# Optimization experiments

Measured on AMD Instinct MI355X. Metric: run time of the kernel, lower is better.

The kernel has to match this reference:

```python
import jax, jax.numpy as jnp
import numpy as np


def setup_inputs() -> dict:
    key = jax.random.key(0)
    k1, k2, k3, k4 = jax.random.split(key, 4)
    B, IN, OUT, K = 1024, 1024, 1024, 100
    return {
        "x": jax.random.normal(k1, (B, IN), dtype=jnp.float32),
        "eps": jax.random.normal(k2, (K, IN, OUT), dtype=jnp.float32),
        "weights_m": jax.random.normal(k3, (IN, OUT), dtype=jnp.float32),
        "weights_s": jax.random.normal(k4, (IN, OUT), dtype=jnp.float32),
    }


def reference(x, eps, weights_m, weights_s):
    # Reparameterized Gaussian weight samples: [K, in, out]
    sampled = eps * jax.nn.softplus(weights_s) + weights_m
    # einsum('ij,kjl->kil'): preds [K, B, out]
    preds = jnp.einsum('ij,kjl->kil', x, sampled)
    return preds.mean(0)
```

## Files before the change

### kernel.cpp

```cpp
#include <hip/hip_runtime.h>
#include <cmath>

#define KSAMP 100
#define DIN   1024
#define DOUT  1024
#define DB    1024

typedef float f4 __attribute__((ext_vector_type(4)));

__global__ __launch_bounds__(256) void weff_kernel(
    const f4* __restrict__ eps,
    const f4* __restrict__ wm,
    const f4* __restrict__ ws,
    f4* __restrict__ weff)
{
    const int idx = blockIdx.x * blockDim.x + threadIdx.x;
    const int n4 = (DIN * DOUT) / 4;

    f4 acc0 = {0.f, 0.f, 0.f, 0.f};
    f4 acc1 = {0.f, 0.f, 0.f, 0.f};
    const f4* p = eps + idx;
    #pragma unroll 10
    for (int k = 0; k < KSAMP; k += 2) {
        f4 e0 = __builtin_nontemporal_load(p);
        f4 e1 = __builtin_nontemporal_load(p + n4);
        p += 2 * n4;
        acc0 += e0;
        acc1 += e1;
    }
    f4 sum = acc0 + acc1;

    f4 s = ws[idx];
    f4 m = wm[idx];
    const float invK = 1.0f / (float)KSAMP;

    f4 sp;
    sp.x = fmaxf(s.x, 0.f) + log1pf(expf(-fabsf(s.x)));
    sp.y = fmaxf(s.y, 0.f) + log1pf(expf(-fabsf(s.y)));
    sp.z = fmaxf(s.z, 0.f) + log1pf(expf(-fabsf(s.z)));
    sp.w = fmaxf(s.w, 0.f) + log1pf(expf(-fabsf(s.w)));

    f4 o;
    o.x = fmaf(sum.x * invK, sp.x, m.x);
    o.y = fmaf(sum.y * invK, sp.y, m.y);
    o.z = fmaf(sum.z * invK, sp.z, m.z);
    o.w = fmaf(sum.w * invK, sp.w, m.w);
    weff[idx] = o;
}

#define BM 128
#define BN 128
#define BK 8
#define KSPLIT 8

__global__ __launch_bounds__(256, 2) void sgemm_splitk(
    const float* __restrict__ A,
    const float* __restrict__ B,
    float* __restrict__ P)
{
    __shared__ float As[BK][BM];
    __shared__ float Bs[BK][BN];

    const int bx = blockIdx.x, by = blockIdx.y, kz = blockIdx.z;
    const int tid = threadIdx.x;
    const int tx = tid & 15;
    const int ty = tid >> 4;

    const int kc = DIN / KSPLIT;
    const int k_begin = kz * kc;

    const int arow = tid >> 1;
    const int acol = (tid & 1) * 4;
    const int brow = tid >> 5;
    const int bcol = (tid & 31) * 4;

    const float* Aptr = &A[(size_t)(by * BM + arow) * DIN + k_begin + acol];
    const float* Bptr = &B[(size_t)(k_begin + brow) * DOUT + bx * BN + bcol];

    float acc[8][8];
    #pragma unroll
    for (int i = 0; i < 8; ++i)
        #pragma unroll
        for (int j = 0; j < 8; ++j) acc[i][j] = 0.f;

    float4 a = *(const float4*)Aptr;
    float4 b = *(const float4*)Bptr;

    const int niter = kc / BK;
    for (int it = 0; it < niter; ++it) {
        __syncthreads();
        As[acol + 0][arow] = a.x;
        As[acol + 1][arow] = a.y;
        As[acol + 2][arow] = a.z;
        As[acol + 3][arow] = a.w;
        *(float4*)&Bs[brow][bcol] = b;
        __syncthreads();

        if (it + 1 < niter) {
            a = *(const float4*)(Aptr + (it + 1) * BK);
            b = *(const float4*)(Bptr + (size_t)(it + 1) * BK * DOUT);
        }

        #pragma unroll
        for (int kk = 0; kk < BK; ++kk) {
            float4 a0 = *(const float4*)&As[kk][ty * 8];
            float4 a1 = *(const float4*)&As[kk][ty * 8 + 4];
            float4 b0 = *(const float4*)&Bs[kk][tx * 8];
            float4 b1 = *(const float4*)&Bs[kk][tx * 8 + 4];
            const float ar[8] = {a0.x, a0.y, a0.z, a0.w, a1.x, a1.y, a1.z, a1.w};
            const float br[8] = {b0.x, b0.y, b0.z, b0.w, b1.x, b1.y, b1.z, b1.w};
            #pragma unroll
            for (int i = 0; i < 8; ++i)
                #pragma unroll
                for (int j = 0; j < 8; ++j)
                    acc[i][j] = fmaf(ar[i], br[j], acc[i][j]);
        }
    }

    float* Pz = P + (size_t)kz * DB * DOUT;
    #pragma unroll
    for (int i = 0; i < 8; ++i) {
        const int r = by * BM + ty * 8 + i;
        float* prow = &Pz[(size_t)r * DOUT + bx * BN + tx * 8];
        *(float4*)&prow[0] = make_float4(acc[i][0], acc[i][1], acc[i][2], acc[i][3]);
        *(float4*)&prow[4] = make_float4(acc[i][4], acc[i][5], acc[i][6], acc[i][7]);
    }
}

__global__ __launch_bounds__(256) void reduce_kernel(
    const f4* __restrict__ P, f4* __restrict__ out)
{
    const int idx = blockIdx.x * blockDim.x + threadIdx.x;
    const int n4 = (DB * DOUT) / 4;
    f4 s = P[idx];
    #pragma unroll
    for (int z = 1; z < KSPLIT; ++z) {
        s += P[(size_t)z * n4 + idx];
    }
    out[idx] = s;
}

extern "C" void kernel_launch(void* const* d_in, const int* in_sizes, int n_in,
                              void* d_out, int out_size, void* d_ws, size_t ws_size,
                              hipStream_t stream) {
    const float* x   = (const float*)d_in[0];
    const float* eps = (const float*)d_in[1];
    const float* wm  = (const float*)d_in[2];
    const float* ws  = (const float*)d_in[3];

    float* weff     = (float*)d_ws;
    float* partials = (float*)d_ws + (size_t)DIN * DOUT;

    weff_kernel<<<(DIN * DOUT / 4) / 256, 256, 0, stream>>>(
        (const f4*)eps, (const f4*)wm, (const f4*)ws, (f4*)weff);

    sgemm_splitk<<<dim3(DOUT / BN, DB / BM, KSPLIT), 256, 0, stream>>>(
        x, weff, partials);

    reduce_kernel<<<(DB * DOUT / 4) / 256, 256, 0, stream>>>(
        (const f4*)partials, (f4*)d_out);
}
```

Measured before the change: 585.5 us.

## Fuse split-K reduction into GEMM via last-block atomic counter, widen BK

Removes the separate reduce kernel. Each GEMM block now bumps a per-tile atomic counter after writing its partial, and the last-arriving block sums the eight partials into the output. The weff kernel resets the counters, and its ws/wm loads are hoisted ahead of the eps loop. BK grows from 8 to 16, and the B-tile columns are split into two 64-wide halves to change the LDS access pattern. This saves a kernel launch and part of the partial traffic, at the cost of a serialized tail reduction done by a few blocks plus threadfence overhead.

Result: slower. 628.7 us (+7.4%).

```diff
diff --git a/kernel.cpp b/kernel.cpp
--- a/kernel.cpp
+++ b/kernel.cpp
@@ -12,10 +12,16 @@
     const f4* __restrict__ eps,
     const f4* __restrict__ wm,
     const f4* __restrict__ ws,
-    f4* __restrict__ weff)
+    f4* __restrict__ weff,
+    int* __restrict__ counters)
 {
     const int idx = blockIdx.x * blockDim.x + threadIdx.x;
     const int n4 = (DIN * DOUT) / 4;
+
+    if (blockIdx.x == 0 && threadIdx.x < 64) counters[threadIdx.x] = 0;
+
+    f4 s = ws[idx];
+    f4 m = wm[idx];
 
     f4 acc0 = {0.f, 0.f, 0.f, 0.f};
     f4 acc1 = {0.f, 0.f, 0.f, 0.f};
@@ -29,9 +35,6 @@
         acc1 += e1;
     }
     f4 sum = acc0 + acc1;
-
-    f4 s = ws[idx];
-    f4 m = wm[idx];
     const float invK = 1.0f / (float)KSAMP;
 
     f4 sp;
@@ -50,13 +53,15 @@
 
 #define BM 128
 #define BN 128
-#define BK 8
+#define BK 16
 #define KSPLIT 8
 
-__global__ __launch_bounds__(256, 2) void sgemm_splitk(
+__global__ __launch_bounds__(256, 2) void sgemm_splitk_fused(
     const float* __restrict__ A,
     const float* __restrict__ B,
-    float* __restrict__ P)
+    float* __restrict__ P,
+    int* __restrict__ counters,
+    float* __restrict__ Out)
 {
     __shared__ float As[BK][BM];
     __shared__ float Bs[BK][BN];
@@ -70,7 +75,7 @@
     const int k_begin = kz * kc;
 
     const int arow = tid >> 1;
-    const int acol = (tid & 1) * 4;
+    const int acol = (tid & 1) * 8;
     const int brow = tid >> 5;
     const int bcol = (tid & 31) * 4;
 
@@ -83,32 +88,41 @@
         #pragma unroll
         for (int j = 0; j < 8; ++j) acc[i][j] = 0.f;
 
-    float4 a = *(const float4*)Aptr;
-    float4 b = *(const float4*)Bptr;
+    float4 a0 = *(const float4*)Aptr;
+    float4 a1 = *(const float4*)(Aptr + 4);
+    float4 b0 = *(const float4*)Bptr;
+    float4 b1 = *(const float4*)(Bptr + 8 * DOUT);
 
     const int niter = kc / BK;
     for (int it = 0; it < niter; ++it) {
         __syncthreads();
-        As[acol + 0][arow] = a.x;
-        As[acol + 1][arow] = a.y;
-        As[acol + 2][arow] = a.z;
-        As[acol + 3][arow] = a.w;
-        *(float4*)&Bs[brow][bcol] = b;
+        As[acol + 0][arow] = a0.x;
+        As[acol + 1][arow] = a0.y;
+        As[acol + 2][arow] = a0.z;
+        As[acol + 3][arow] = a0.w;
+        As[acol + 4][arow] = a1.x;
+        As[acol + 5][arow] = a1.y;
+        As[acol + 6][arow] = a1.z;
+        As[acol + 7][arow] = a1.w;
+        *(float4*)&Bs[brow][bcol]     = b0;
+        *(float4*)&Bs[brow + 8][bcol] = b1;
         __syncthreads();
 
         if (it + 1 < niter) {
-            a = *(const float4*)(Aptr + (it + 1) * BK);
-            b = *(const float4*)(Bptr + (size_t)(it + 1) * BK * DOUT);
+            a0 = *(const float4*)(Aptr + (it + 1) * BK);
+            a1 = *(const float4*)(Aptr + (it + 1) * BK + 4);
+            b0 = *(const float4*)(Bptr + (size_t)((it + 1) * BK) * DOUT);
+            b1 = *(const float4*)(Bptr + (size_t)((it + 1) * BK + 8) * DOUT);
         }
 
         #pragma unroll
         for (int kk = 0; kk < BK; ++kk) {
-            float4 a0 = *(const float4*)&As[kk][ty * 8];
-            float4 a1 = *(const float4*)&As[kk][ty * 8 + 4];
-            float4 b0 = *(const float4*)&Bs[kk][tx * 8];
-            float4 b1 = *(const float4*)&Bs[kk][tx * 8 + 4];
-            const float ar[8] = {a0.x, a0.y, a0.z, a0.w, a1.x, a1.y, a1.z, a1.w};
-            const float br[8] = {b0.x, b0.y, b0.z, b0.w, b1.x, b1.y, b1.z, b1.w};
+            float4 A0 = *(const float4*)&As[kk][ty * 8];
+            float4 A1 = *(const float4*)&As[kk][ty * 8 + 4];
+            float4 B0 = *(const float4*)&Bs[kk][tx * 4];
+            float4 B1 = *(const float4*)&Bs[kk][64 + tx * 4];
+            const float ar[8] = {A0.x, A0.y, A0.z, A0.w, A1.x, A1.y, A1.z, A1.w};
+            const float br[8] = {B0.x, B0.y, B0.z, B0.w, B1.x, B1.y, B1.z, B1.w};
             #pragma unroll
             for (int i = 0; i < 8; ++i)
                 #pragma unroll
@@ -121,23 +135,36 @@
     #pragma unroll
     for (int i = 0; i < 8; ++i) {
         const int r = by * BM + ty * 8 + i;
-        float* prow = &Pz[(size_t)r * DOUT + bx * BN + tx * 8];
-        *(float4*)&prow[0] = make_float4(acc[i][0], acc[i][1], acc[i][2], acc[i][3]);
-        *(float4*)&prow[4] = make_float4(acc[i][4], acc[i][5], acc[i][6], acc[i][7]);
+        float* prow = &Pz[(size_t)r * DOUT + bx * BN];
+        *(f4*)&prow[tx * 4]      = (f4){acc[i][0], acc[i][1], acc[i][2], acc[i][3]};
+        *(f4*)&prow[64 + tx * 4] = (f4){acc[i][4], acc[i][5], acc[i][6], acc[i][7]};
     }
-}
 
-__global__ __launch_bounds__(256) void reduce_kernel(
-    const f4* __restrict__ P, f4* __restrict__ out)
-{
-    const int idx = blockIdx.x * blockDim.x + threadIdx.x;
-    const int n4 = (DB * DOUT) / 4;
-    f4 s = P[idx];
-    #pragma unroll
-    for (int z = 1; z < KSPLIT; ++z) {
-        s += P[(size_t)z * n4 + idx];
+    __threadfence();
+    __shared__ int isLast;
+    if (tid == 0) {
+        int prev = atomicAdd(&counters[by * 8 + bx], 1);
+        isLast = (prev == KSPLIT - 1) ? 1 : 0;
     }
-    out[idx] = s;
+    __syncthreads();
+    if (isLast) {
+        __threadfence();
+        #pragma unroll
+        for (int i = 0; i < 8; ++i) {
+            const int r = by * BM + ty * 8 + i;
+            const size_t rowoff = (size_t)r * DOUT + bx * BN;
+            f4 s0 = {0.f, 0.f, 0.f, 0.f};
+            f4 s1 = {0.f, 0.f, 0.f, 0.f};
+            #pragma unroll
+            for (int z = 0; z < KSPLIT; ++z) {
+                const float* pz = P + (size_t)z * DB * DOUT + rowoff;
+                s0 += *(const f4*)&pz[tx * 4];
+                s1 += *(const f4*)&pz[64 + tx * 4];
+            }
+            *(f4*)&Out[rowoff + tx * 4]      = s0;
+            *(f4*)&Out[rowoff + 64 + tx * 4] = s1;
+        }
+    }
 }
 
 extern "C" void kernel_launch(void* const* d_in, const int* in_sizes, int n_in,
@@ -150,13 +177,12 @@
 
     float* weff     = (float*)d_ws;
     float* partials = (float*)d_ws + (size_t)DIN * DOUT;
+    int*   counters = (int*)((float*)d_ws + (size_t)DIN * DOUT
+                             + (size_t)KSPLIT * DB * DOUT);
 
     weff_kernel<<<(DIN * DOUT / 4) / 256, 256, 0, stream>>>(
-        (const f4*)eps, (const f4*)wm, (const f4*)ws, (f4*)weff);
+        (const f4*)eps, (const f4*)wm, (const f4*)ws, (f4*)weff, counters);
 
-    sgemm_splitk<<<dim3(DOUT / BN, DB / BM, KSPLIT), 256, 0, stream>>>(
-        x, weff, partials);
-
-    reduce_kernel<<<(DB * DOUT / 4) / 256, 256, 0, stream>>>(
-        (const f4*)partials, (f4*)d_out);
+    sgemm_splitk_fused<<<dim3(DOUT / BN, DB / BM, KSPLIT), 256, 0, stream>>>(
+        x, weff, partials, counters, (float*)d_out);
 }
```
